# Kernel tuning notes

Measured on AMD Instinct MI355X. Metric: run time of the kernel, lower is better.

Reference implementation:

```python
import jax, jax.numpy as jnp
import numpy as np

# Model hyperparameters (Mamba(dim=256, expand=1, d_state=16, bimamba_type='v2'))
D_MODEL = 256      # dim; expand=1 -> d_inner = D_MODEL
D_STATE = 16
DT_RANK = 16       # ceil(256/16)
D_CONV = 4
BATCH = 2
SEQ = 4096         # H*W = 64*64


def _ln(x, g, b, eps=1e-5):
    m = jnp.mean(x, axis=-1, keepdims=True)
    v = jnp.mean((x - m) ** 2, axis=-1, keepdims=True)
    return (x - m) * jax.lax.rsqrt(v + eps) * g + b


def _causal_dwconv(x, w, b):
    # x: [B, L, d], w: [d, 1, K] (depthwise), causal padding K-1 on the left
    xt = jnp.transpose(x, (0, 2, 1))  # [B, d, L]
    y = jax.lax.conv_general_dilated(
        xt, w, window_strides=(1,), padding=[(w.shape[-1] - 1, 0)],
        dimension_numbers=('NCH', 'OIH', 'NCH'), feature_group_count=xt.shape[1])
    return jnp.transpose(y + b[None, :, None], (0, 2, 1))


def _selective_scan(u, dt, Bm, Cm, A, D, z):
    # u, dt, z: [B, L, d]; Bm, Cm: [B, L, N]; A: [d, N]; D: [d]
    def step(h, inp):
        dt_t, B_t, C_t, u_t = inp            # [B,d], [B,N], [B,N], [B,d]
        h = h * jnp.exp(dt_t[:, :, None] * A) + (dt_t * u_t)[:, :, None] * B_t[:, None, :]
        y = jnp.einsum('bdn,bn->bd', h, C_t)
        return h, y

    h0 = jnp.zeros((u.shape[0], u.shape[2], A.shape[1]), u.dtype)
    xs = (jnp.transpose(dt, (1, 0, 2)), jnp.transpose(Bm, (1, 0, 2)),
          jnp.transpose(Cm, (1, 0, 2)), jnp.transpose(u, (1, 0, 2)))
    _, ys = jax.lax.scan(step, h0, xs)       # ys: [L, B, d]
    y = jnp.transpose(ys, (1, 0, 2)) + u * D
    return y * jax.nn.silu(z)                # SiLU(z) gating (done inside mamba_inner_fn)


def _mamba_dir(xin, z, conv_w, conv_b, xproj_w, dtproj_w, dtproj_b, A_log, D):
    u = jax.nn.silu(_causal_dwconv(xin, conv_w, conv_b))
    dbl = u @ xproj_w.T                       # [B, L, dt_rank + 2*N]
    dt = dbl[..., :DT_RANK]
    Bm = dbl[..., DT_RANK:DT_RANK + D_STATE]
    Cm = dbl[..., DT_RANK + D_STATE:]
    dt = jax.nn.softplus(dt @ dtproj_w.T + dtproj_b)
    return _selective_scan(u, dt, Bm, Cm, -jnp.exp(A_log), D, z)


def setup_inputs() -> dict:
    key = jax.random.key(0)
    ks = jax.random.split(key, 24)
    d, N, R, K = D_MODEL, D_STATE, DT_RANK, D_CONV
    s = 0.02
    A_log = jnp.log(jnp.tile(jnp.arange(1, N + 1, dtype=jnp.float32)[None, :], (d, 1)))
    return {
        'input': jax.random.normal(ks[0], (BATCH, SEQ, d), jnp.float32),
        'norm_g': jnp.ones((d,), jnp.float32),
        'norm_b': jnp.zeros((d,), jnp.float32),
        'in_proj_w': jax.random.normal(ks[1], (2 * d, d), jnp.float32) * s,
        # forward-direction SSM params
        'conv_w': jax.random.normal(ks[2], (d, 1, K), jnp.float32) * 0.1,
        'conv_b': jnp.zeros((d,), jnp.float32),
        'xproj_w': jax.random.normal(ks[3], (R + 2 * N, d), jnp.float32) * s,
        'dtproj_w': jax.random.normal(ks[4], (d, R), jnp.float32) * 0.1,
        'dtproj_b': jax.random.normal(ks[5], (d,), jnp.float32) * 0.1 - 4.0,
        'A_log': A_log,
        'Dp': jnp.ones((d,), jnp.float32),
        # backward-direction SSM params (bimamba v2)
        'conv_w_b': jax.random.normal(ks[6], (d, 1, K), jnp.float32) * 0.1,
        'conv_b_b': jnp.zeros((d,), jnp.float32),
        'xproj_w_b': jax.random.normal(ks[7], (R + 2 * N, d), jnp.float32) * s,
        'dtproj_w_b': jax.random.normal(ks[8], (d, R), jnp.float32) * 0.1,
        'dtproj_b_b': jax.random.normal(ks[9], (d,), jnp.float32) * 0.1 - 4.0,
        'A_log_b': A_log,
        'Dp_b': jnp.ones((d,), jnp.float32),
        # pre-out_proj norm (use_norm=True) and out projection
        'out_norm_g': jnp.ones((d,), jnp.float32),
        'out_norm_b': jnp.zeros((d,), jnp.float32),
        'out_proj_w': jax.random.normal(ks[10], (d, d), jnp.float32) * s,
        'post_norm_g': jnp.ones((d,), jnp.float32),
        'post_norm_b': jnp.zeros((d,), jnp.float32),
    }


def reference(input, norm_g, norm_b, in_proj_w,
              conv_w, conv_b, xproj_w, dtproj_w, dtproj_b, A_log, Dp,
              conv_w_b, conv_b_b, xproj_w_b, dtproj_w_b, dtproj_b_b, A_log_b, Dp_b,
              out_norm_g, out_norm_b, out_proj_w, post_norm_g, post_norm_b):
    skip = input
    x = _ln(input, norm_g, norm_b)
    xz = x @ in_proj_w.T                      # [B, L, 2d]
    xin, z = jnp.split(xz, 2, axis=-1)
    # forward direction
    y_f = _mamba_dir(xin, z, conv_w, conv_b, xproj_w, dtproj_w, dtproj_b, A_log, Dp)
    # backward direction: flip sequence, run, flip back
    y_b = _mamba_dir(xin[:, ::-1], z[:, ::-1], conv_w_b, conv_b_b, xproj_w_b,
                     dtproj_w_b, dtproj_b_b, A_log_b, Dp_b)[:, ::-1]
    y = (y_f + y_b) * 0.5                     # if_devide_out=True
    y = _ln(y, out_norm_g, out_norm_b)        # use_norm=True
    out = y @ out_proj_w.T
    out = _ln(out, post_norm_g, post_norm_b)
    return out + skip
```

## Files before the change

### kernel.cpp

```cpp
#include <hip/hip_runtime.h>
#include <math.h>

#define DM 256
#define SQ 4096
#define BT 2
#define NS 16
#define NTOK (BT*SQ)
#define NCHK 128
#define CHL (SQ/NCHK)

typedef __attribute__((ext_vector_type(8))) short short8;
typedef __attribute__((ext_vector_type(4))) float f32x4;

__device__ __forceinline__ float sigm_(float x){ return 1.f/(1.f+__expf(-x)); }
__device__ __forceinline__ float silu_(float x){ return x*sigm_(x); }
__device__ __forceinline__ float softplus_(float x){ return (x>20.f)? x : log1pf(__expf(x)); }
__device__ __forceinline__ unsigned short f2bf(float f){
  unsigned int u = __float_as_uint(f);
  unsigned int r = (u + 0x7FFFu + ((u>>16)&1u)) >> 16;
  return (unsigned short)r;
}
__device__ __forceinline__ float bf2f(unsigned short u){
  return __uint_as_float(((unsigned int)u)<<16);
}

__global__ __launch_bounds__(256) void k_prep(
    const float* __restrict__ x, const float* __restrict__ g, const float* __restrict__ nb,
    unsigned short* __restrict__ xl,
    const float* __restrict__ Win, unsigned short* __restrict__ Wbin,
    const float* __restrict__ xw_f, const float* __restrict__ xw_b,
    const float* __restrict__ dtw_f, const float* __restrict__ dtw_b,
    unsigned short* __restrict__ Wcatb,
    const float* __restrict__ Wout, unsigned short* __restrict__ Wbout)
{
  int bx = blockIdx.x;
  int tid = threadIdx.x;
  if (bx < NTOK/4){
    int tok = bx*4 + (tid>>6);
    int lane = tid & 63;
    const float* row = x + (size_t)tok*DM;
    float4 v = *(const float4*)(row + lane*4);
    float s = v.x+v.y+v.z+v.w;
    float ss = v.x*v.x+v.y*v.y+v.z*v.z+v.w*v.w;
    #pragma unroll
    for (int o=32;o>0;o>>=1){ s += __shfl_xor(s,o,64); ss += __shfl_xor(ss,o,64); }
    float m = s*(1.f/DM);
    float r = rsqrtf(ss*(1.f/DM)-m*m+1e-5f);
    float4 gv = *(const float4*)(g + lane*4);
    float4 bv = *(const float4*)(nb + lane*4);
    ushort4 o4;
    o4.x = f2bf((v.x-m)*r*gv.x+bv.x);
    o4.y = f2bf((v.y-m)*r*gv.y+bv.y);
    o4.z = f2bf((v.z-m)*r*gv.z+bv.z);
    o4.w = f2bf((v.w-m)*r*gv.w+bv.w);
    *(ushort4*)(xl + (size_t)tok*DM + lane*4) = o4;
  } else if (bx < NTOK/4 + 128){
    int i = ((bx - NTOK/4)*256 + tid)*4;
    float4 v = *(const float4*)(Win + i);
    ushort4 o4; o4.x=f2bf(v.x); o4.y=f2bf(v.y); o4.z=f2bf(v.z); o4.w=f2bf(v.w);
    *(ushort4*)(Wbin + i) = o4;
  } else if (bx < NTOK/4 + 136){
    int idx = bx - (NTOK/4 + 128);
    int dir = idx >> 2;
    int kc = (idx & 3)*64;
    const float* xw  = dir? xw_b : xw_f;
    const float* dtw = dir? dtw_b : dtw_f;
    int d = tid;
    float dw[16];
    #pragma unroll
    for (int r=0;r<16;r++) dw[r] = dtw[d*16+r];
    unsigned short* Wd = Wcatb + (size_t)dir*320*DM + (size_t)d*DM + kc;
    for (int kk=0;kk<64;kk++){
      float acc = 0.f;
      #pragma unroll
      for (int r=0;r<16;r++) acc += dw[r]*xw[r*DM + kc + kk];
      Wd[kk] = f2bf(acc);
    }
    if (d < 64){
      unsigned short* Wr = Wcatb + (size_t)dir*320*DM + (size_t)(256+d)*DM + kc;
      if (d < 32){
        const float* src = xw + (size_t)(16+d)*DM + kc;
        for (int kk=0;kk<64;kk++) Wr[kk] = f2bf(src[kk]);
      } else {
        for (int kk=0;kk<64;kk++) Wr[kk] = 0;
      }
    }
  } else {
    int i = ((bx - (NTOK/4 + 136))*256 + tid)*4;
    float4 v = *(const float4*)(Wout + i);
    ushort4 o4; o4.x=f2bf(v.x); o4.y=f2bf(v.y); o4.z=f2bf(v.z); o4.w=f2bf(v.w);
    *(ushort4*)(Wbout + i) = o4;
  }
}

__global__ __launch_bounds__(256) void k_inproj_conv(
    const unsigned short* __restrict__ xl, const unsigned short* __restrict__ Wb,
    const float* __restrict__ cw_f, const float* __restrict__ cb_f,
    const float* __restrict__ cw_b, const float* __restrict__ cb_b,
    unsigned short* __restrict__ ufb, unsigned short* __restrict__ ubb,
    unsigned short* __restrict__ zb)
{
  __shared__ float xs[134][68];
  __shared__ unsigned short xh[6][256];
  int tid = threadIdx.x;
  int wid = tid >> 6, lane = tid & 63;
  int wm = wid >> 1, wn = wid & 1;
  int row0 = blockIdx.x*128 + wm*64;
  int col0 = blockIdx.y*64 + wn*32;
  int lr = lane & 15, lg = lane >> 4;
  f32x4 acc[4][2];
  #pragma unroll
  for (int m=0;m<4;m++)
    #pragma unroll
    for (int n=0;n<2;n++) acc[m][n] = (f32x4){0.f,0.f,0.f,0.f};

  #pragma unroll
  for (int k0=0;k0<DM;k0+=32){
    short8 a[4], b[2];
    #pragma unroll
    for (int m=0;m<4;m++)
      a[m] = *(const short8*)(xl + (size_t)(row0 + m*16 + lr)*DM + k0 + lg*8);
    #pragma unroll
    for (int n=0;n<2;n++)
      b[n] = *(const short8*)(Wb + (size_t)(col0 + n*16 + lr)*DM + k0 + lg*8);
    #pragma unroll
    for (int m=0;m<4;m++)
      #pragma unroll
      for (int n=0;n<2;n++)
        acc[m][n] = __builtin_amdgcn_mfma_f32_16x16x32_bf16(a[m], b[n], acc[m][n], 0,0,0);
  }
  if (blockIdx.y >= 4){
    int cb = col0 - 256;
    #pragma unroll
    for (int m=0;m<4;m++)
      #pragma unroll
      for (int n=0;n<2;n++)
        #pragma unroll
        for (int r=0;r<4;r++){
          int rr = row0 + m*16 + lg*4 + r;
          int cc = cb + n*16 + lr;
          zb[(size_t)rr*DM + cc] = f2bf(acc[m][n][r]);
        }
    return;
  }
  #pragma unroll
  for (int m=0;m<4;m++)
    #pragma unroll
    for (int n=0;n<2;n++)
      #pragma unroll
      for (int r=0;r<4;r++)
        xs[wm*64 + m*16 + lg*4 + r + 3][wn*32 + n*16 + lr] = acc[m][n][r];
  int b_  = blockIdx.x >> 5;
  int lt0 = (blockIdx.x & 31)*128;
  for (int i=tid; i<6*256; i+=256){
    int hr = i >> 8, k = i & 255;
    int lt = (hr<3)? (lt0-3+hr) : (lt0+128+(hr-3));
    unsigned short v = 0;
    if (lt >= 0 && lt < SQ) v = xl[((size_t)b_*SQ+lt)*DM + k];
    xh[hr][k] = v;
  }
  __syncthreads();
  for (int i=tid; i<384; i+=256){
    int hr = i >> 6, col = i & 63;
    int gcol = blockIdx.y*64 + col;
    float acch = 0.f;
    for (int k=0;k<256;k+=8){
      short8 xa = *(const short8*)&xh[hr][k];
      short8 wv = *(const short8*)(Wb + (size_t)gcol*DM + k);
      #pragma unroll
      for (int e=0;e<8;e++) acch += bf2f((unsigned short)xa[e])*bf2f((unsigned short)wv[e]);
    }
    int xr = (hr<3)? hr : (131 + hr - 3);
    xs[xr][col] = acch;
  }
  __syncthreads();
  int col = tid & 63, tg = tid >> 6;
  int gd = blockIdx.y*64 + col;
  float wf0=cw_f[gd*4], wf1=cw_f[gd*4+1], wf2=cw_f[gd*4+2], wf3=cw_f[gd*4+3];
  float wb0=cw_b[gd*4], wb1=cw_b[gd*4+1], wb2=cw_b[gd*4+2], wb3=cw_b[gd*4+3];
  float bfv = cb_f[gd], bbv = cb_b[gd];
  for (int i=0;i<32;i++){
    int r = tg*32 + i;
    float x0=xs[r][col], x1=xs[r+1][col], x2=xs[r+2][col], x3=xs[r+3][col];
    float vf = silu_(bfv + wf0*x0 + wf1*x1 + wf2*x2 + wf3*x3);
    ufb[((size_t)b_*SQ + lt0 + r)*DM + gd] = f2bf(vf);
    float x4=xs[r+4][col], x5=xs[r+5][col], x6=xs[r+6][col];
    float vb = silu_(bbv + wb3*x3 + wb2*x4 + wb1*x5 + wb0*x6);
    ubb[((size_t)b_*SQ + (SQ-1-(lt0+r)))*DM + gd] = f2bf(vb);
  }
}

__global__ __launch_bounds__(256) void k_xproj_mfma(
    const unsigned short* __restrict__ ufb, const unsigned short* __restrict__ ubb,
    const unsigned short* __restrict__ Wcatb,
    const float* __restrict__ dtbias_f, const float* __restrict__ dtbias_b,
    unsigned short* __restrict__ dt16f, unsigned short* __restrict__ dt16b,
    float* __restrict__ bmf, float* __restrict__ cmf,
    float* __restrict__ bmb, float* __restrict__ cmb)
{
  int dir = blockIdx.z;
  const unsigned short* u  = dir? ubb : ufb;
  const unsigned short* Wc = Wcatb + (size_t)dir*320*DM;
  const float* dbi = dir? dtbias_b : dtbias_f;
  unsigned short* dt = dir? dt16b : dt16f;
  float* bm = dir? bmb : bmf;
  float* cm = dir? cmb : cmf;
  int tid = threadIdx.x;
  int wid = tid >> 6, lane = tid & 63;
  int wm = wid >> 1, wn = wid & 1;
  int row0 = blockIdx.x*128 + wm*64;
  int col0 = blockIdx.y*64 + wn*32;
  int lr = lane & 15, lg = lane >> 4;
  f32x4 acc[4][2];
  #pragma unroll
  for (int m=0;m<4;m++)
    #pragma unroll
    for (int n=0;n<2;n++) acc[m][n] = (f32x4){0.f,0.f,0.f,0.f};
  #pragma unroll
  for (int k0=0;k0<DM;k0+=32){
    short8 a[4], b[2];
    #pragma unroll
    for (int m=0;m<4;m++)
      a[m] = *(const short8*)(u + (size_t)(row0 + m*16 + lr)*DM + k0 + lg*8);
    #pragma unroll
    for (int n=0;n<2;n++)
      b[n] = *(const short8*)(Wc + (size_t)(col0 + n*16 + lr)*DM + k0 + lg*8);
    #pragma unroll
    for (int m=0;m<4;m++)
      #pragma unroll
      for (int n=0;n<2;n++)
        acc[m][n] = __builtin_amdgcn_mfma_f32_16x16x32_bf16(a[m], b[n], acc[m][n], 0,0,0);
  }
  if (blockIdx.y < 4){
    #pragma unroll
    for (int n=0;n<2;n++){
      int cc = col0 + n*16 + lr;
      float bias = dbi[cc];
      #pragma unroll
      for (int m=0;m<4;m++)
        #pragma unroll
        for (int r=0;r<4;r++){
          int rr = row0 + m*16 + lg*4 + r;
          dt[(size_t)rr*DM + cc] = f2bf(softplus_(acc[m][n][r] + bias));
        }
    }
  } else if (wn == 0){
    #pragma unroll
    for (int n=0;n<2;n++){
      float* outp = n ? cm : bm;
      #pragma unroll
      for (int m=0;m<4;m++)
        #pragma unroll
        for (int r=0;r<4;r++){
          int rr = row0 + m*16 + lg*4 + r;
          outp[(size_t)rr*NS + lr] = acc[m][n][r];
        }
    }
  }
}

__global__ __launch_bounds__(256) void k_scan1(
    const unsigned short* __restrict__ dtf, const unsigned short* __restrict__ dtb,
    const unsigned short* __restrict__ ufb, const unsigned short* __restrict__ ubb,
    const float* __restrict__ bmf, const float* __restrict__ bmb,
    const float* __restrict__ alog_f, const float* __restrict__ alog_b,
    float* __restrict__ apf, float* __restrict__ hsf,
    float* __restrict__ apb, float* __restrict__ hsb)
{
  int c = blockIdx.x, b = blockIdx.y, dir = blockIdx.z;
  const unsigned short* dt = dir? dtb : dtf;
  const unsigned short* u  = dir? ubb : ufb;
  const float* bmp= dir? bmb : bmf;
  const float* al = dir? alog_b : alog_f;
  float* ap = dir? apb : apf;
  float* hs = dir? hsb : hsf;
  int d = threadIdx.x;
  __shared__ float sB[CHL*NS];
  for (int i=threadIdx.x;i<CHL*NS;i+=256) sB[i] = bmp[((size_t)b*SQ + c*CHL)*NS + i];
  float A[NS];
  #pragma unroll
  for (int n=0;n<NS;n++) A[n] = -__expf(al[d*NS+n]);
  float h[NS] = {};
  float dts = 0.f;
  __syncthreads();
  for (int t=0;t<CHL;t++){
    size_t idx = ((size_t)b*SQ + c*CHL + t)*DM + d;
    float dtv = bf2f(dt[idx]);
    float uv  = bf2f(u[idx]);
    float du  = dtv*uv;
    dts += dtv;
    #pragma unroll
    for (int n=0;n<NS;n++) h[n] = h[n]*__expf(dtv*A[n]) + du*sB[t*NS+n];
  }
  size_t o = (((size_t)b*NCHK + c)*DM + d)*NS;
  #pragma unroll
  for (int n=0;n<NS;n++){ hs[o+n] = h[n]; ap[o+n] = __expf(A[n]*dts); }
}

__global__ __launch_bounds__(256) void k_scan2(
    float* __restrict__ apf, float* __restrict__ hsf,
    float* __restrict__ apb, float* __restrict__ hsb)
{
  __shared__ float sa[NCHK][64];
  __shared__ float sv[NCHK][64];
  __shared__ float segA[4][64], segV[4][64];
  int bx = blockIdx.x;
  int dg = bx & 63, b = (bx>>6)&1, dir = bx>>7;
  const float* ap = dir? apb : apf;
  float* hs = dir? hsb : hsf;
  int dn = threadIdx.x & 63;
  int cg = threadIdx.x >> 6;
  size_t base = (size_t)b*NCHK*4096 + dg*64 + dn;
  for (int i=0;i<32;i++){
    int c = cg*32 + i;
    size_t idx = base + (size_t)c*4096;
    sa[c][dn] = ap[idx];
    sv[c][dn] = hs[idx];
  }
  __syncthreads();
  float A = 1.f, V = 0.f;
  for (int i=0;i<32;i++){
    int c = cg*32 + i;
    float a = sa[c][dn], v = sv[c][dn];
    V = a*V + v;
    A = A*a;
  }
  segA[cg][dn] = A; segV[cg][dn] = V;
  __syncthreads();
  float pre = 0.f;
  for (int s=0;s<cg;s++) pre = segA[s][dn]*pre + segV[s][dn];
  float xv = pre;
  for (int i=0;i<32;i++){
    int c = cg*32 + i;
    size_t idx = base + (size_t)c*4096;
    hs[idx] = xv;
    float a = sa[c][dn], v = sv[c][dn];
    xv = a*xv + v;
  }
}

__global__ __launch_bounds__(256) void k_scan3(
    const unsigned short* __restrict__ dtf, const unsigned short* __restrict__ dtb,
    const unsigned short* __restrict__ ufb, const unsigned short* __restrict__ ubb,
    const float* __restrict__ bmf, const float* __restrict__ bmb,
    const float* __restrict__ cmf, const float* __restrict__ cmb,
    const float* __restrict__ alf, const float* __restrict__ alb,
    const float* __restrict__ Df, const float* __restrict__ Db,
    const unsigned short* __restrict__ zb,
    const float* __restrict__ hsf, const float* __restrict__ hsb,
    unsigned short* __restrict__ yf, unsigned short* __restrict__ yb)
{
  int c = blockIdx.x, b = blockIdx.y;
  int dir = blockIdx.z;
  const unsigned short* dt = dir? dtb : dtf;
  const unsigned short* u  = dir? ubb : ufb;
  const float* bmp= dir? bmb : bmf;
  const float* cmp= dir? cmb : cmf;
  const float* al = dir? alb : alf;
  const float* Dv = dir? Db  : Df;
  const float* hs = dir? hsb : hsf;
  unsigned short* yout = dir? yb : yf;
  int d = threadIdx.x;
  __shared__ float sB[CHL*NS];
  __shared__ float sC[CHL*NS];
  for (int i=threadIdx.x;i<CHL*NS;i+=256){
    sB[i] = bmp[((size_t)b*SQ + c*CHL)*NS + i];
    sC[i] = cmp[((size_t)b*SQ + c*CHL)*NS + i];
  }
  float A[NS], h[NS];
  size_t o = (((size_t)b*NCHK + c)*DM + d)*NS;
  #pragma unroll
  for (int n=0;n<NS;n++){ A[n] = -__expf(al[d*NS+n]); h[n] = hs[o+n]; }
  float Dd = Dv[d];
  __syncthreads();
  for (int t=0;t<CHL;t++){
    int gt = c*CHL + t;
    size_t idx = ((size_t)b*SQ + gt)*DM + d;
    float dtv = bf2f(dt[idx]);
    float uv  = bf2f(u[idx]);
    float du  = dtv*uv;
    float y = 0.f;
    #pragma unroll
    for (int n=0;n<NS;n++){
      h[n] = h[n]*__expf(dtv*A[n]) + du*sB[t*NS+n];
      y += h[n]*sC[t*NS+n];
    }
    y += uv*Dd;
    int torig = dir ? (SQ-1-gt) : gt;
    size_t oidx = ((size_t)b*SQ + torig)*DM + d;
    float zv = bf2f(zb[oidx]);
    yout[oidx] = f2bf(y * (zv * sigm_(zv)));
  }
}

#define SOS 266
__global__ __launch_bounds__(256) void k_final2(
    const unsigned short* __restrict__ y16f, const unsigned short* __restrict__ y16b,
    const float* __restrict__ og, const float* __restrict__ ob,
    const unsigned short* __restrict__ Wb,
    const float* __restrict__ pg, const float* __restrict__ pb,
    const float* __restrict__ skip, float* __restrict__ out)
{
  __shared__ unsigned short yn[32][272];
  __shared__ float sOut[32*SOS];
  __shared__ float sm[32], sr[32];
  int tid = threadIdx.x;
  int wid = tid >> 6, lane = tid & 63;
  int row0 = blockIdx.x*32;
  for (int j=0;j<8;j++){
    int rrow = wid*8 + j;
    size_t base = (size_t)(row0+rrow)*DM + lane*4;
    ushort4 hf = *(const ushort4*)(y16f + base);
    ushort4 hb = *(const ushort4*)(y16b + base);
    float4 v;
    v.x = 0.5f*(bf2f(hf.x)+bf2f(hb.x));
    v.y = 0.5f*(bf2f(hf.y)+bf2f(hb.y));
    v.z = 0.5f*(bf2f(hf.z)+bf2f(hb.z));
    v.w = 0.5f*(bf2f(hf.w)+bf2f(hb.w));
    float s = v.x+v.y+v.z+v.w;
    float ss = v.x*v.x+v.y*v.y+v.z*v.z+v.w*v.w;
    #pragma unroll
    for (int o=32;o>0;o>>=1){ s += __shfl_xor(s,o,64); ss += __shfl_xor(ss,o,64); }
    float m = s*(1.f/DM);
    float r = rsqrtf(ss*(1.f/DM)-m*m+1e-5f);
    float4 gv = *(const float4*)(og + lane*4);
    float4 bv = *(const float4*)(ob + lane*4);
    ushort4 o4;
    o4.x = f2bf((v.x-m)*r*gv.x+bv.x);
    o4.y = f2bf((v.y-m)*r*gv.y+bv.y);
    o4.z = f2bf((v.z-m)*r*gv.z+bv.z);
    o4.w = f2bf((v.w-m)*r*gv.w+bv.w);
    *(ushort4*)&yn[rrow][lane*4] = o4;
  }
  __syncthreads();
  int lr = lane & 15, lg = lane >> 4;
  int col0 = wid*64;
  f32x4 acc[2][4];
  #pragma unroll
  for (int m=0;m<2;m++)
    #pragma unroll
    for (int n=0;n<4;n++) acc[m][n] = (f32x4){0.f,0.f,0.f,0.f};
  #pragma unroll
  for (int k0=0;k0<DM;k0+=32){
    short8 a[2], b[4];
    #pragma unroll
    for (int m=0;m<2;m++)
      a[m] = *(const short8*)&yn[m*16 + lr][k0 + lg*8];
    #pragma unroll
    for (int n=0;n<4;n++)
      b[n] = *(const short8*)(Wb + (size_t)(col0 + n*16 + lr)*DM + k0 + lg*8);
    #pragma unroll
    for (int m=0;m<2;m++)
      #pragma unroll
      for (int n=0;n<4;n++)
        acc[m][n] = __builtin_amdgcn_mfma_f32_16x16x32_bf16(a[m], b[n], acc[m][n], 0,0,0);
  }
  #pragma unroll
  for (int m=0;m<2;m++)
    #pragma unroll
    for (int n=0;n<4;n++)
      #pragma unroll
      for (int r=0;r<4;r++)
        sOut[(m*16 + lg*4 + r)*SOS + col0 + n*16 + lr] = acc[m][n][r];
  __syncthreads();
  for (int j=0;j<8;j++){
    int rrow = wid*8 + j;
    const float* rp = &sOut[rrow*SOS + lane*4];
    float2 v0 = *(const float2*)(rp);
    float2 v1 = *(const float2*)(rp+2);
    float s = v0.x+v0.y+v1.x+v1.y;
    float ss = v0.x*v0.x+v0.y*v0.y+v1.x*v1.x+v1.y*v1.y;
    #pragma unroll
    for (int o=32;o>0;o>>=1){ s += __shfl_xor(s,o,64); ss += __shfl_xor(ss,o,64); }
    if (lane==0){ float m=s*(1.f/DM); sm[rrow]=m; sr[rrow]=rsqrtf(ss*(1.f/DM)-m*m+1e-5f); }
  }
  __syncthreads();
  float gv = pg[tid], bv = pb[tid];
  for (int rrow=0;rrow<32;rrow++){
    int tok = row0 + rrow;
    float v = (sOut[rrow*SOS + tid]-sm[rrow])*sr[rrow]*gv + bv + skip[(size_t)tok*DM + tid];
    out[(size_t)tok*DM + tid] = v;
  }
}

extern "C" void kernel_launch(void* const* d_in, const int* in_sizes, int n_in,
                              void* d_out, int out_size, void* d_ws, size_t ws_size,
                              hipStream_t stream)
{
  const float* input      = (const float*)d_in[0];
  const float* norm_g     = (const float*)d_in[1];
  const float* norm_b     = (const float*)d_in[2];
  const float* in_proj_w  = (const float*)d_in[3];
  const float* conv_w     = (const float*)d_in[4];
  const float* conv_b     = (const float*)d_in[5];
  const float* xproj_w    = (const float*)d_in[6];
  const float* dtproj_w   = (const float*)d_in[7];
  const float* dtproj_b   = (const float*)d_in[8];
  const float* A_log      = (const float*)d_in[9];
  const float* Dp         = (const float*)d_in[10];
  const float* conv_w_b   = (const float*)d_in[11];
  const float* conv_b_b   = (const float*)d_in[12];
  const float* xproj_w_b  = (const float*)d_in[13];
  const float* dtproj_w_b = (const float*)d_in[14];
  const float* dtproj_b_b = (const float*)d_in[15];
  const float* A_log_b    = (const float*)d_in[16];
  const float* Dp_b       = (const float*)d_in[17];
  const float* out_norm_g = (const float*)d_in[18];
  const float* out_norm_b = (const float*)d_in[19];
  const float* out_proj_w = (const float*)d_in[20];
  const float* post_norm_g= (const float*)d_in[21];
  const float* post_norm_b= (const float*)d_in[22];
  float* out = (float*)d_out;

  float* ws = (float*)d_ws;
  const size_t M2 = (size_t)NTOK*DM;
  const size_t SCH = (size_t)BT*NCHK*DM*NS;
  unsigned short* y16f = (unsigned short*)ws;
  unsigned short* y16b = (unsigned short*)ws + M2;
  unsigned short* zbuf = (unsigned short*)(ws + M2);
  unsigned short* auxw = (unsigned short*)(ws + M2 + M2/2);
  unsigned short* Wbin  = auxw;
  unsigned short* Wcatb = auxw + 131072;
  unsigned short* Wbout = auxw + 131072 + 163840;
  unsigned short* dt16f = (unsigned short*)(ws + 3*M2);
  unsigned short* dt16b = dt16f + M2;
  unsigned short* ufb = (unsigned short*)(ws + 4*M2);
  unsigned short* ubb = ufb + M2;
  float* p   = ws + 5*M2;
  float* bmf = p;              p += (size_t)NTOK*NS;
  float* cmf = p;              p += (size_t)NTOK*NS;
  float* bmb = p;              p += (size_t)NTOK*NS;
  float* cmb = p;              p += (size_t)NTOK*NS;
  float* apf = p;              p += SCH;
  float* hsf = p;              p += SCH;
  float* apb = p;              p += SCH;
  float* hsb = p;              p += SCH;
  unsigned short* xlbf = (unsigned short*)apf;

  k_prep<<<NTOK/4 + 136 + 64, 256, 0, stream>>>(input, norm_g, norm_b, xlbf,
                                                in_proj_w, Wbin,
                                                xproj_w, xproj_w_b, dtproj_w, dtproj_w_b, Wcatb,
                                                out_proj_w, Wbout);
  k_inproj_conv<<<dim3(NTOK/128, 8, 1), 256, 0, stream>>>(xlbf, Wbin,
                                                          conv_w, conv_b, conv_w_b, conv_b_b,
                                                          ufb, ubb, zbuf);
  k_xproj_mfma<<<dim3(NTOK/128, 5, 2), 256, 0, stream>>>(ufb, ubb, Wcatb,
                                                         dtproj_b, dtproj_b_b,
                                                         dt16f, dt16b, bmf, cmf, bmb, cmb);
  k_scan1<<<dim3(NCHK, BT, 2), 256, 0, stream>>>(dt16f, dt16b, ufb, ubb, bmf, bmb,
                                                 A_log, A_log_b, apf, hsf, apb, hsb);
  k_scan2<<<256, 256, 0, stream>>>(apf, hsf, apb, hsb);
  k_scan3<<<dim3(NCHK, BT, 2), 256, 0, stream>>>(dt16f, dt16b, ufb, ubb, bmf, bmb, cmf, cmb,
                                                 A_log, A_log_b, Dp, Dp_b, zbuf, hsf, hsb,
                                                 y16f, y16b);
  k_final2<<<NTOK/32, 256, 0, stream>>>(y16f, y16b, out_norm_g, out_norm_b, Wbout,
                                        post_norm_g, post_norm_b, input, out);
}
```

Measured before the change: 144.4 us.

## Store per-chunk dt sums instead of decay products and prefetch scan inputs

```diff
diff --git a/kernel.cpp b/kernel.cpp
--- a/kernel.cpp
+++ b/kernel.cpp
@@ -8,6 +8,7 @@
 #define NTOK (BT*SQ)
 #define NCHK 128
 #define CHL (SQ/NCHK)
+#define LOG2E 1.4426950408889634f
 
 typedef __attribute__((ext_vector_type(8))) short short8;
 typedef __attribute__((ext_vector_type(4))) float f32x4;
@@ -264,77 +265,80 @@
     const unsigned short* __restrict__ ufb, const unsigned short* __restrict__ ubb,
     const float* __restrict__ bmf, const float* __restrict__ bmb,
     const float* __restrict__ alog_f, const float* __restrict__ alog_b,
-    float* __restrict__ apf, float* __restrict__ hsf,
-    float* __restrict__ apb, float* __restrict__ hsb)
+    float* __restrict__ dtsf, float* __restrict__ hsf,
+    float* __restrict__ dtsb, float* __restrict__ hsb)
 {
   int c = blockIdx.x, b = blockIdx.y, dir = blockIdx.z;
   const unsigned short* dt = dir? dtb : dtf;
   const unsigned short* u  = dir? ubb : ufb;
   const float* bmp= dir? bmb : bmf;
   const float* al = dir? alog_b : alog_f;
-  float* ap = dir? apb : apf;
+  float* dts_out = dir? dtsb : dtsf;
   float* hs = dir? hsb : hsf;
   int d = threadIdx.x;
   __shared__ float sB[CHL*NS];
   for (int i=threadIdx.x;i<CHL*NS;i+=256) sB[i] = bmp[((size_t)b*SQ + c*CHL)*NS + i];
-  float A[NS];
-  #pragma unroll
-  for (int n=0;n<NS;n++) A[n] = -__expf(al[d*NS+n]);
+  float A2[NS];
+  #pragma unroll
+  for (int n=0;n<NS;n++) A2[n] = -__expf(al[d*NS+n])*LOG2E;
   float h[NS] = {};
   float dts = 0.f;
   __syncthreads();
+  size_t idx = ((size_t)b*SQ + c*CHL)*DM + d;
+  unsigned short dtr = dt[idx], ur = u[idx];
   for (int t=0;t<CHL;t++){
-    size_t idx = ((size_t)b*SQ + c*CHL + t)*DM + d;
-    float dtv = bf2f(dt[idx]);
-    float uv  = bf2f(u[idx]);
+    unsigned short dtn=0, un=0;
+    if (t+1 < CHL){ dtn = dt[idx+DM]; un = u[idx+DM]; }
+    float dtv = bf2f(dtr);
+    float uv  = bf2f(ur);
     float du  = dtv*uv;
     dts += dtv;
     #pragma unroll
-    for (int n=0;n<NS;n++) h[n] = h[n]*__expf(dtv*A[n]) + du*sB[t*NS+n];
+    for (int n=0;n<NS;n++) h[n] = h[n]*exp2f(dtv*A2[n]) + du*sB[t*NS+n];
+    dtr = dtn; ur = un; idx += DM;
   }
   size_t o = (((size_t)b*NCHK + c)*DM + d)*NS;
   #pragma unroll
-  for (int n=0;n<NS;n++){ hs[o+n] = h[n]; ap[o+n] = __expf(A[n]*dts); }
+  for (int n=0;n<NS;n++) hs[o+n] = h[n];
+  dts_out[((size_t)b*NCHK + c)*DM + d] = dts;
 }
 
 __global__ __launch_bounds__(256) void k_scan2(
-    float* __restrict__ apf, float* __restrict__ hsf,
-    float* __restrict__ apb, float* __restrict__ hsb)
-{
-  __shared__ float sa[NCHK][64];
-  __shared__ float sv[NCHK][64];
-  __shared__ float segA[4][64], segV[4][64];
-  int bx = blockIdx.x;
-  int dg = bx & 63, b = (bx>>6)&1, dir = bx>>7;
-  const float* ap = dir? apb : apf;
+    const float* __restrict__ dtsf, float* __restrict__ hsf,
+    const float* __restrict__ dtsb, float* __restrict__ hsb,
+    const float* __restrict__ alog_f, const float* __restrict__ alog_b)
+{
+  __shared__ float segA[8][32], segV[8][32];
+  int b = blockIdx.y, dir = blockIdx.z;
+  const float* dts = dir? dtsb : dtsf;
   float* hs = dir? hsb : hsf;
-  int dn = threadIdx.x & 63;
-  int cg = threadIdx.x >> 6;
-  size_t base = (size_t)b*NCHK*4096 + dg*64 + dn;
-  for (int i=0;i<32;i++){
-    int c = cg*32 + i;
+  const float* al = dir? alog_b : alog_f;
+  int tid = threadIdx.x;
+  int chain = blockIdx.x*32 + (tid & 31);
+  int seg = tid >> 5;
+  int dch = chain >> 4;
+  float A2 = -__expf(al[chain])*LOG2E;
+  size_t base = (size_t)b*NCHK*4096 + chain;
+  size_t dbase = (size_t)b*NCHK*DM + dch;
+  float Ac = 1.f, Vc = 0.f;
+  for (int i=0;i<16;i++){
+    int c = seg*16 + i;
+    float a = exp2f(A2*dts[dbase + (size_t)c*DM]);
+    float v = hs[base + (size_t)c*4096];
+    Vc = a*Vc + v;
+    Ac = Ac*a;
+  }
+  segA[seg][tid&31] = Ac; segV[seg][tid&31] = Vc;
+  __syncthreads();
+  float pre = 0.f;
+  for (int s=0;s<seg;s++) pre = segA[s][tid&31]*pre + segV[s][tid&31];
+  float xv = pre;
+  for (int i=0;i<16;i++){
+    int c = seg*16 + i;
     size_t idx = base + (size_t)c*4096;
-    sa[c][dn] = ap[idx];
-    sv[c][dn] = hs[idx];
-  }
-  __syncthreads();
-  float A = 1.f, V = 0.f;
-  for (int i=0;i<32;i++){
-    int c = cg*32 + i;
-    float a = sa[c][dn], v = sv[c][dn];
-    V = a*V + v;
-    A = A*a;
-  }
-  segA[cg][dn] = A; segV[cg][dn] = V;
-  __syncthreads();
-  float pre = 0.f;
-  for (int s=0;s<cg;s++) pre = segA[s][dn]*pre + segV[s][dn];
-  float xv = pre;
-  for (int i=0;i<32;i++){
-    int c = cg*32 + i;
-    size_t idx = base + (size_t)c*4096;
+    float a = exp2f(A2*dts[dbase + (size_t)c*DM]);
+    float v = hs[idx];
     hs[idx] = xv;
-    float a = sa[c][dn], v = sv[c][dn];
     xv = a*xv + v;
   }
 }
@@ -367,29 +371,36 @@
     sB[i] = bmp[((size_t)b*SQ + c*CHL)*NS + i];
     sC[i] = cmp[((size_t)b*SQ + c*CHL)*NS + i];
   }
-  float A[NS], h[NS];
+  float A2[NS], h[NS];
   size_t o = (((size_t)b*NCHK + c)*DM + d)*NS;
   #pragma unroll
-  for (int n=0;n<NS;n++){ A[n] = -__expf(al[d*NS+n]); h[n] = hs[o+n]; }
+  for (int n=0;n<NS;n++){ A2[n] = -__expf(al[d*NS+n])*LOG2E; h[n] = hs[o+n]; }
   float Dd = Dv[d];
   __syncthreads();
+  int t0g = c*CHL;
+  size_t idx = ((size_t)b*SQ + t0g)*DM + d;
+  long zstep = dir ? -(long)DM : (long)DM;
+  size_t zidx = ((size_t)b*SQ + (dir ? (SQ-1-t0g) : t0g))*DM + d;
+  unsigned short dtr = dt[idx], ur = u[idx], zr = zb[zidx];
   for (int t=0;t<CHL;t++){
-    int gt = c*CHL + t;
-    size_t idx = ((size_t)b*SQ + gt)*DM + d;
-    float dtv = bf2f(dt[idx]);
-    float uv  = bf2f(u[idx]);
+    unsigned short dtn=0, un=0, zn=0;
+    if (t+1 < CHL){
+      dtn = dt[idx+DM]; un = u[idx+DM]; zn = zb[zidx+zstep];
+    }
+    float dtv = bf2f(dtr);
+    float uv  = bf2f(ur);
     float du  = dtv*uv;
     float y = 0.f;
     #pragma unroll
     for (int n=0;n<NS;n++){
-      h[n] = h[n]*__expf(dtv*A[n]) + du*sB[t*NS+n];
+      h[n] = h[n]*exp2f(dtv*A2[n]) + du*sB[t*NS+n];
       y += h[n]*sC[t*NS+n];
     }
     y += uv*Dd;
-    int torig = dir ? (SQ-1-gt) : gt;
-    size_t oidx = ((size_t)b*SQ + torig)*DM + d;
-    float zv = bf2f(zb[oidx]);
-    yout[oidx] = f2bf(y * (zv * sigm_(zv)));
+    float zv = bf2f(zr);
+    yout[zidx] = f2bf(y * (zv * sigm_(zv)));
+    dtr = dtn; ur = un; zr = zn;
+    idx += DM; zidx += zstep;
   }
 }
 
@@ -531,11 +542,11 @@
   float* cmf = p;              p += (size_t)NTOK*NS;
   float* bmb = p;              p += (size_t)NTOK*NS;
   float* cmb = p;              p += (size_t)NTOK*NS;
-  float* apf = p;              p += SCH;
+  float* dtsf = p;             p += (size_t)BT*NCHK*DM;
+  float* dtsb = p;             p += (size_t)BT*NCHK*DM;
   float* hsf = p;              p += SCH;
-  float* apb = p;              p += SCH;
   float* hsb = p;              p += SCH;
-  unsigned short* xlbf = (unsigned short*)apf;
+  unsigned short* xlbf = (unsigned short*)hsf;
 
   k_prep<<<NTOK/4 + 136 + 64, 256, 0, stream>>>(input, norm_g, norm_b, xlbf,
                                                 in_proj_w, Wbin,
@@ -548,8 +559,8 @@
                                                          dtproj_b, dtproj_b_b,
                                                          dt16f, dt16b, bmf, cmf, bmb, cmb);
   k_scan1<<<dim3(NCHK, BT, 2), 256, 0, stream>>>(dt16f, dt16b, ufb, ubb, bmf, bmb,
-                                                 A_log, A_log_b, apf, hsf, apb, hsb);
-  k_scan2<<<256, 256, 0, stream>>>(apf, hsf, apb, hsb);
+                                                 A_log, A_log_b, dtsf, hsf, dtsb, hsb);
+  k_scan2<<<dim3(DM*NS/32, BT, 2), 256, 0, stream>>>(dtsf, hsf, dtsb, hsb, A_log, A_log_b);
   k_scan3<<<dim3(NCHK, BT, 2), 256, 0, stream>>>(dt16f, dt16b, ufb, ubb, bmf, bmb, cmf, cmb,
                                                  A_log, A_log_b, Dp, Dp_b, zbuf, hsf, hsb,
                                                  y16f, y16b);
```

After: 150.2 us. 1.04x slower.
